# Optimization experiments

Hardware: AMD Instinct MI355X
Metric: run time of the kernel (lower is better)

## Reference

```python
import jax, jax.numpy as jnp
import numpy as np

N = 100000   # nodes
E = 1600000  # edges (before self-loops)
IN = 128     # in_features
H = 4        # heads
C = 64       # out_features per head
D = H * C    # concat output dim = 256
NEG_SLOPE = 0.2
EPS = 1e-5


def setup_inputs() -> dict:
    key = jax.random.key(0)
    k = jax.random.split(key, 8)
    x = jax.random.normal(k[0], (N, IN), jnp.float32)
    edge_index = jax.random.randint(k[1], (2, E), 0, N, jnp.int32)
    # GATConv params (glorot-ish init)
    W = jax.random.normal(k[2], (IN, D), jnp.float32) * np.float32(np.sqrt(2.0 / (IN + D)))
    att_src = jax.random.normal(k[3], (H, C), jnp.float32) * np.float32(np.sqrt(2.0 / C))
    att_dst = jax.random.normal(k[4], (H, C), jnp.float32) * np.float32(np.sqrt(2.0 / C))
    bias = jnp.zeros((D,), jnp.float32)
    # LayerNorm params
    gamma = jnp.ones((D,), jnp.float32)
    beta = jnp.zeros((D,), jnp.float32)
    return {"x": x, "edge_index": edge_index, "W": W, "att_src": att_src,
            "att_dst": att_dst, "bias": bias, "gamma": gamma, "beta": beta}


def reference(x, edge_index, W, att_src, att_dst, bias, gamma, beta):
    # --- GATConv (add_self_loops=True, negative_slope=0.2, eval-mode dropout) ---
    loops = jnp.arange(N, dtype=edge_index.dtype)
    ei = jnp.concatenate([edge_index, jnp.stack([loops, loops])], axis=1)  # (2, E+N)
    src, dst = ei[0], ei[1]

    h = (x @ W).reshape(N, H, C)                       # (N,H,C)
    a_s = jnp.einsum('nhc,hc->nh', h, att_src)          # (N,H)
    a_d = jnp.einsum('nhc,hc->nh', h, att_dst)          # (N,H)

    logits = jax.nn.leaky_relu(a_s[src] + a_d[dst], NEG_SLOPE)  # (Etot,H)
    # segment softmax over incoming edges of each destination node
    mx = jax.ops.segment_max(logits, dst, num_segments=N)       # (N,H)
    ex = jnp.exp(logits - mx[dst])
    den = jax.ops.segment_sum(ex, dst, num_segments=N)          # (N,H)
    alpha = ex / den[dst]                                       # (Etot,H)

    msg = h[src] * alpha[:, :, None]                             # (Etot,H,C)
    out = jax.ops.segment_sum(msg, dst, num_segments=N)          # (N,H,C)
    out = out.reshape(N, D) + bias

    # --- ELU + LayerNorm (dropout = identity in eval) ---
    out = jax.nn.elu(out)
    mu = out.mean(-1, keepdims=True)
    var = out.var(-1, keepdims=True)
    out = (out - mu) * jax.lax.rsqrt(var + EPS) * gamma + beta
    return out
```

## Files before the change

### kernel.cpp

```cpp
#include <hip/hip_runtime.h>
#include <hip/hip_bf16.h>

#define IN_F 128
#define DF   256
#define NEG  0.2f
#define LN_EPS 1e-5f

typedef __attribute__((ext_vector_type(8))) short bf16x8;
typedef __attribute__((ext_vector_type(4))) float f32x4;

__device__ __forceinline__ float lrelu(float x) { return x > 0.f ? x : NEG * x; }
__device__ __forceinline__ float b2f(unsigned short u) {
    union { unsigned int i; float f; } v; v.i = ((unsigned int)u) << 16; return v.f;
}
__device__ __forceinline__ unsigned short f2b(float f) {
    union { float f; unsigned int i; } v; v.f = f;
    unsigned int r = v.i + 0x7FFFu + ((v.i >> 16) & 1u);
    return (unsigned short)(r >> 16);
}

__global__ __launch_bounds__(256) void k_pack(const float* __restrict__ W,
                                              unsigned short* __restrict__ Wp)
{
    int t = blockIdx.x * 256 + threadIdx.x;
    if (t >= 16 * 4 * 64) return;
    int lane = t & 63, ks = (t >> 6) & 3, ct = t >> 8;
    int col = ct * 16 + (lane & 15);
    int kb  = ks * 32 + (lane >> 4) * 8;
    unsigned short* dst = Wp + (size_t)t * 8;
    #pragma unroll
    for (int j = 0; j < 8; ++j)
        dst[j] = f2b(W[(size_t)(kb + j) * DF + col]);
}

#define APAD 136
__global__ __launch_bounds__(256) void k_gemm(
        const float* __restrict__ x, const unsigned short* __restrict__ Wp,
        unsigned short* __restrict__ hb, int N)
{
    __shared__ unsigned short lds_a[64 * APAD];
    int t = threadIdx.x;
    int row0 = blockIdx.x * 64;

    const float4* xg = (const float4*)x;
    #pragma unroll
    for (int j = 0; j < 8; ++j) {
        int s = t + j * 256;
        int r = s >> 5, c4 = s & 31;
        ushort4 w = make_ushort4(0, 0, 0, 0);
        if (row0 + r < N) {
            float4 xv = xg[(size_t)(row0 + r) * 32 + c4];
            w = make_ushort4(f2b(xv.x), f2b(xv.y), f2b(xv.z), f2b(xv.w));
        }
        *(ushort4*)(&lds_a[r * APAD + c4 * 4]) = w;
    }
    __syncthreads();

    int lane = t & 63, wid = t >> 6;
    int rbase = (wid & 1) * 32;
    int cbase = (wid >> 1) * 128;
    int ct0 = cbase >> 4;

    bf16x8 af[2][4];
    #pragma unroll
    for (int rt = 0; rt < 2; ++rt)
        #pragma unroll
        for (int ks = 0; ks < 4; ++ks) {
            int r = rbase + rt * 16 + (lane & 15);
            int k = ks * 32 + (lane >> 4) * 8;
            af[rt][ks] = *(const bf16x8*)(&lds_a[r * APAD + k]);
        }

    f32x4 acc[2][8];
    #pragma unroll
    for (int rt = 0; rt < 2; ++rt)
        #pragma unroll
        for (int ct = 0; ct < 8; ++ct)
            acc[rt][ct] = (f32x4){0.f, 0.f, 0.f, 0.f};

    const bf16x8* Wp8 = (const bf16x8*)Wp;
    #pragma unroll
    for (int ct = 0; ct < 8; ++ct) {
        #pragma unroll
        for (int ks = 0; ks < 4; ++ks) {
            bf16x8 b = Wp8[((ct0 + ct) * 4 + ks) * 64 + lane];
            acc[0][ct] = __builtin_amdgcn_mfma_f32_16x16x32_bf16(af[0][ks], b, acc[0][ct], 0, 0, 0);
            acc[1][ct] = __builtin_amdgcn_mfma_f32_16x16x32_bf16(af[1][ks], b, acc[1][ct], 0, 0, 0);
        }
    }

    #pragma unroll
    for (int rt = 0; rt < 2; ++rt) {
        #pragma unroll
        for (int ct = 0; ct < 8; ++ct) {
            int col = cbase + ct * 16 + (lane & 15);
            #pragma unroll
            for (int r = 0; r < 4; ++r) {
                int row = row0 + rbase + rt * 16 + (lane >> 4) * 4 + r;
                if (row < N)
                    hb[(size_t)row * DF + col] = f2b(acc[rt][ct][r]);
            }
        }
    }
}

__global__ __launch_bounds__(256) void k_att(
        const unsigned short* __restrict__ hb,
        const float* __restrict__ att_s, const float* __restrict__ att_d,
        float* __restrict__ a_s, float* __restrict__ a_d, int N)
{
    int wid = threadIdx.x >> 6, lane = threadIdx.x & 63;
    int n = blockIdx.x * 4 + wid;
    if (n >= N) return;
    int d0 = lane << 2, head = lane >> 4;
    ushort4 hv = *(const ushort4*)(hb + (size_t)n * DF + d0);
    float4 as4 = *(const float4*)(att_s + d0);
    float4 ad4 = *(const float4*)(att_d + d0);
    float h0 = b2f(hv.x), h1 = b2f(hv.y), h2 = b2f(hv.z), h3 = b2f(hv.w);
    float vs = h0 * as4.x + h1 * as4.y + h2 * as4.z + h3 * as4.w;
    float vd = h0 * ad4.x + h1 * ad4.y + h2 * ad4.z + h3 * ad4.w;
    #pragma unroll
    for (int m = 8; m >= 1; m >>= 1) {
        vs += __shfl_xor(vs, m, 64);
        vd += __shfl_xor(vd, m, 64);
    }
    if ((lane & 15) == 0) {
        a_s[(size_t)n * 4 + head] = vs;
        a_d[(size_t)n * 4 + head] = vd;
    }
}

__global__ void k_count(const int* __restrict__ dste, int E, int* __restrict__ indeg)
{
    for (int e = blockIdx.x * blockDim.x + threadIdx.x; e < E; e += gridDim.x * blockDim.x)
        atomicAdd(&indeg[dste[e]], 1);
}

__global__ __launch_bounds__(256) void k_scanA(const int* __restrict__ indeg, int N, int* __restrict__ part)
{
    int t = threadIdx.x, base = blockIdx.x * 1024;
    int s = 0;
    #pragma unroll
    for (int j = 0; j < 4; ++j) { int i = base + t * 4 + j; if (i < N) s += indeg[i]; }
    #pragma unroll
    for (int m = 32; m >= 1; m >>= 1) s += __shfl_xor(s, m, 64);
    __shared__ int red[4];
    if ((t & 63) == 0) red[t >> 6] = s;
    __syncthreads();
    if (t == 0) part[blockIdx.x] = red[0] + red[1] + red[2] + red[3];
}

__global__ __launch_bounds__(128) void k_scanB(const int* __restrict__ part, int NB, int* __restrict__ bloff)
{
    __shared__ int buf[128];
    int t = threadIdx.x;
    int v = (t < NB) ? part[t] : 0;
    buf[t] = v;
    __syncthreads();
    for (int off = 1; off < 128; off <<= 1) {
        int x2 = (t >= off) ? buf[t - off] : 0;
        __syncthreads();
        buf[t] += x2;
        __syncthreads();
    }
    if (t < NB) bloff[t] = buf[t] - v;
}

__global__ __launch_bounds__(256) void k_scanC(const int* __restrict__ indeg, int N,
        const int* __restrict__ bloff, int* __restrict__ offs, int* __restrict__ cur)
{
    int t = threadIdx.x, bid = blockIdx.x, base = bid * 1024;
    int v[4]; int s = 0;
    #pragma unroll
    for (int j = 0; j < 4; ++j) { int i = base + t * 4 + j; v[j] = (i < N) ? indeg[i] : 0; s += v[j]; }
    __shared__ int lds[256];
    lds[t] = s;
    __syncthreads();
    for (int off = 1; off < 256; off <<= 1) {
        int x2 = (t >= off) ? lds[t - off] : 0;
        __syncthreads();
        lds[t] += x2;
        __syncthreads();
    }
    int run = lds[t] - s + bloff[bid];
    #pragma unroll
    for (int j = 0; j < 4; ++j) {
        int i = base + t * 4 + j;
        if (i < N) { offs[i] = run; cur[i] = run; }
        run += v[j];
    }
    if (bid == (int)gridDim.x - 1 && t == 255) offs[N] = run;
}

__global__ void k_scatter(const int* __restrict__ srce, const int* __restrict__ dste, int E,
                          int* __restrict__ cur, int* __restrict__ srclist)
{
    for (int e = blockIdx.x * blockDim.x + threadIdx.x; e < E; e += gridDim.x * blockDim.x) {
        int d = dste[e];
        int p = atomicAdd(&cur[d], 1);
        srclist[p] = srce[e];
    }
}

__global__ __launch_bounds__(256) void k_gather(
        const unsigned short* __restrict__ hb,
        const float* __restrict__ a_s, const float* __restrict__ a_d,
        const int* __restrict__ offs, const int* __restrict__ srclist,
        const float* __restrict__ bias, const float* __restrict__ gamma,
        const float* __restrict__ beta, float* __restrict__ out, int N)
{
    int wid = threadIdx.x >> 6, lane = threadIdx.x & 63;
    int n = blockIdx.x * 4 + wid;
    if (n >= N) return;
    int head = lane >> 4;
    int d0 = lane << 2;

    float adh = a_d[(size_t)n * 4 + head];
    int beg = offs[n], end = offs[n + 1];

    float acc0, acc1, acc2, acc3, den;
    {
        float as = a_s[(size_t)n * 4 + head];
        float p = expf(lrelu(as + adh));
        den = p;
        ushort4 hv = *(const ushort4*)(hb + (size_t)n * DF + d0);
        acc0 = p * b2f(hv.x); acc1 = p * b2f(hv.y);
        acc2 = p * b2f(hv.z); acc3 = p * b2f(hv.w);
    }

    int e = beg;
    int s_next = (e < end) ? srclist[e] : 0;
    while (e < end) {
        int s = s_next;
        ++e;
        if (e < end) s_next = srclist[e];
        float as = a_s[(size_t)s * 4 + head];
        ushort4 hv = *(const ushort4*)(hb + (size_t)s * DF + d0);
        float p = expf(lrelu(as + adh));
        den += p;
        acc0 = fmaf(p, b2f(hv.x), acc0); acc1 = fmaf(p, b2f(hv.y), acc1);
        acc2 = fmaf(p, b2f(hv.z), acc2); acc3 = fmaf(p, b2f(hv.w), acc3);
    }

    float inv = 1.f / den;
    float4 bia = *(const float4*)(bias + d0);
    float v0 = fmaf(acc0, inv, bia.x);
    float v1 = fmaf(acc1, inv, bia.y);
    float v2 = fmaf(acc2, inv, bia.z);
    float v3 = fmaf(acc3, inv, bia.w);
    v0 = v0 > 0.f ? v0 : expm1f(v0);
    v1 = v1 > 0.f ? v1 : expm1f(v1);
    v2 = v2 > 0.f ? v2 : expm1f(v2);
    v3 = v3 > 0.f ? v3 : expm1f(v3);

    float s1 = v0 + v1 + v2 + v3;
    float s2 = v0 * v0 + v1 * v1 + v2 * v2 + v3 * v3;
    #pragma unroll
    for (int m = 32; m >= 1; m >>= 1) {
        s1 += __shfl_xor(s1, m, 64);
        s2 += __shfl_xor(s2, m, 64);
    }
    float mu = s1 * (1.f / 256.f);
    float var = s2 * (1.f / 256.f) - mu * mu;
    float rs = rsqrtf(var + LN_EPS);
    float4 g  = *(const float4*)(gamma + d0);
    float4 be = *(const float4*)(beta + d0);
    float4 o;
    o.x = (v0 - mu) * rs * g.x + be.x;
    o.y = (v1 - mu) * rs * g.y + be.y;
    o.z = (v2 - mu) * rs * g.z + be.z;
    o.w = (v3 - mu) * rs * g.w + be.w;
    *(float4*)(out + (size_t)n * DF + d0) = o;
}

extern "C" void kernel_launch(void* const* d_in, const int* in_sizes, int n_in,
                              void* d_out, int out_size, void* d_ws, size_t ws_size,
                              hipStream_t stream)
{
    const float* x     = (const float*)d_in[0];
    const int*   ei    = (const int*)d_in[1];
    const float* W     = (const float*)d_in[2];
    const float* att_s = (const float*)d_in[3];
    const float* att_d = (const float*)d_in[4];
    const float* bias  = (const float*)d_in[5];
    const float* gamma = (const float*)d_in[6];
    const float* beta  = (const float*)d_in[7];
    float* out = (float*)d_out;

    int N = in_sizes[0] / IN_F;
    int E = in_sizes[1] / 2;
    const int* srce = ei;
    const int* dste = ei + E;

    char* wsb = (char*)d_ws;
    size_t off = 0;
    auto alloc = [&](size_t bytes) -> void* {
        void* p = wsb + off;
        off += (bytes + 255) & ~(size_t)255;
        return p;
    };
    unsigned short* hb = (unsigned short*)alloc((size_t)N * DF * sizeof(unsigned short));
    unsigned short* Wp = (unsigned short*)alloc((size_t)IN_F * DF * sizeof(unsigned short));
    float* a_s   = (float*)alloc((size_t)N * 4 * sizeof(float));
    float* a_d   = (float*)alloc((size_t)N * 4 * sizeof(float));
    int*   indeg = (int*)alloc((size_t)N * sizeof(int));
    int*   offs  = (int*)alloc(((size_t)N + 1) * sizeof(int));
    int*   cur   = (int*)alloc((size_t)N * sizeof(int));
    int*   srclist = (int*)alloc((size_t)E * sizeof(int));
    int NB = (N + 1023) / 1024;
    int* part  = (int*)alloc((size_t)NB * sizeof(int));
    int* bloff = (int*)alloc((size_t)NB * sizeof(int));

    (void)hipMemsetAsync(indeg, 0, (size_t)N * sizeof(int), stream);

    k_pack<<<16, 256, 0, stream>>>(W, Wp);
    k_gemm<<<(N + 63) / 64, 256, 0, stream>>>(x, Wp, hb, N);
    k_att<<<(N + 3) / 4, 256, 0, stream>>>(hb, att_s, att_d, a_s, a_d, N);
    k_count<<<2048, 256, 0, stream>>>(dste, E, indeg);
    k_scanA<<<NB, 256, 0, stream>>>(indeg, N, part);
    k_scanB<<<1, 128, 0, stream>>>(part, NB, bloff);
    k_scanC<<<NB, 256, 0, stream>>>(indeg, N, bloff, offs, cur);
    k_scatter<<<2048, 256, 0, stream>>>(srce, dste, E, cur, srclist);
    k_gather<<<(N + 3) / 4, 256, 0, stream>>>(hb, a_s, a_d, offs, srclist, bias, gamma, beta, out, N);
}
```

Before: 527.0 us.

## Batch edge logits across lanes and switch h storage to fp16

The gather kernel now handles incoming edges in batches of 16. Each lane loads one source index and computes its attention weight with fast __expf, then broadcasts the index and weight via shuffles for the feature accumulation, and the denominator is reduced with xor-shuffles. This removes the serial dependent index loads and the per-edge exp computed redundantly by every lane. The intermediate h buffer moves from bf16 to fp16, which gives more mantissa precision at the same size and changes the conversion instructions. The trade-off is extra shuffle traffic and lower occupancy in partial batches for low-degree nodes.

```diff
diff --git a/kernel.cpp b/kernel.cpp
--- a/kernel.cpp
+++ b/kernel.cpp
@@ -8,11 +8,10 @@
 
 typedef __attribute__((ext_vector_type(8))) short bf16x8;
 typedef __attribute__((ext_vector_type(4))) float f32x4;
+typedef _Float16 f16;
+typedef __attribute__((ext_vector_type(4))) _Float16 f16x4;
 
 __device__ __forceinline__ float lrelu(float x) { return x > 0.f ? x : NEG * x; }
-__device__ __forceinline__ float b2f(unsigned short u) {
-    union { unsigned int i; float f; } v; v.i = ((unsigned int)u) << 16; return v.f;
-}
 __device__ __forceinline__ unsigned short f2b(float f) {
     union { float f; unsigned int i; } v; v.f = f;
     unsigned int r = v.i + 0x7FFFu + ((v.i >> 16) & 1u);
@@ -36,7 +35,7 @@
 #define APAD 136
 __global__ __launch_bounds__(256) void k_gemm(
         const float* __restrict__ x, const unsigned short* __restrict__ Wp,
-        unsigned short* __restrict__ hb, int N)
+        f16* __restrict__ hb, int N)
 {
     __shared__ unsigned short lds_a[64 * APAD];
     int t = threadIdx.x;
@@ -98,14 +97,14 @@
             for (int r = 0; r < 4; ++r) {
                 int row = row0 + rbase + rt * 16 + (lane >> 4) * 4 + r;
                 if (row < N)
-                    hb[(size_t)row * DF + col] = f2b(acc[rt][ct][r]);
+                    hb[(size_t)row * DF + col] = (f16)acc[rt][ct][r];
             }
         }
     }
 }
 
 __global__ __launch_bounds__(256) void k_att(
-        const unsigned short* __restrict__ hb,
+        const f16* __restrict__ hb,
         const float* __restrict__ att_s, const float* __restrict__ att_d,
         float* __restrict__ a_s, float* __restrict__ a_d, int N)
 {
@@ -113,10 +112,10 @@
     int n = blockIdx.x * 4 + wid;
     if (n >= N) return;
     int d0 = lane << 2, head = lane >> 4;
-    ushort4 hv = *(const ushort4*)(hb + (size_t)n * DF + d0);
+    f16x4 hv = *(const f16x4*)(hb + (size_t)n * DF + d0);
     float4 as4 = *(const float4*)(att_s + d0);
     float4 ad4 = *(const float4*)(att_d + d0);
-    float h0 = b2f(hv.x), h1 = b2f(hv.y), h2 = b2f(hv.z), h3 = b2f(hv.w);
+    float h0 = (float)hv.x, h1 = (float)hv.y, h2 = (float)hv.z, h3 = (float)hv.w;
     float vs = h0 * as4.x + h1 * as4.y + h2 * as4.z + h3 * as4.w;
     float vd = h0 * ad4.x + h1 * ad4.y + h2 * ad4.z + h3 * ad4.w;
     #pragma unroll
@@ -203,7 +202,7 @@
 }
 
 __global__ __launch_bounds__(256) void k_gather(
-        const unsigned short* __restrict__ hb,
+        const f16* __restrict__ hb,
         const float* __restrict__ a_s, const float* __restrict__ a_d,
         const int* __restrict__ offs, const int* __restrict__ srclist,
         const float* __restrict__ bias, const float* __restrict__ gamma,
@@ -213,34 +212,43 @@
     int n = blockIdx.x * 4 + wid;
     if (n >= N) return;
     int head = lane >> 4;
+    int j16  = lane & 15;
     int d0 = lane << 2;
 
     float adh = a_d[(size_t)n * 4 + head];
     int beg = offs[n], end = offs[n + 1];
 
-    float acc0, acc1, acc2, acc3, den;
+    float acc0, acc1, acc2, acc3;
+    float den = 0.f;
     {
         float as = a_s[(size_t)n * 4 + head];
-        float p = expf(lrelu(as + adh));
-        den = p;
-        ushort4 hv = *(const ushort4*)(hb + (size_t)n * DF + d0);
-        acc0 = p * b2f(hv.x); acc1 = p * b2f(hv.y);
-        acc2 = p * b2f(hv.z); acc3 = p * b2f(hv.w);
-    }
-
-    int e = beg;
-    int s_next = (e < end) ? srclist[e] : 0;
-    while (e < end) {
-        int s = s_next;
-        ++e;
-        if (e < end) s_next = srclist[e];
+        float p = __expf(lrelu(as + adh));
+        if (j16 == 0) den = p;
+        f16x4 hv = *(const f16x4*)(hb + (size_t)n * DF + d0);
+        acc0 = p * (float)hv.x; acc1 = p * (float)hv.y;
+        acc2 = p * (float)hv.z; acc3 = p * (float)hv.w;
+    }
+
+    for (int tb = beg; tb < end; tb += 16) {
+        int nb = end - tb; nb = nb > 16 ? 16 : nb;
+        int   s = (j16 < nb) ? srclist[tb + j16] : 0;
         float as = a_s[(size_t)s * 4 + head];
-        ushort4 hv = *(const ushort4*)(hb + (size_t)s * DF + d0);
-        float p = expf(lrelu(as + adh));
+        float p  = (j16 < nb) ? __expf(lrelu(as + adh)) : 0.f;
         den += p;
-        acc0 = fmaf(p, b2f(hv.x), acc0); acc1 = fmaf(p, b2f(hv.y), acc1);
-        acc2 = fmaf(p, b2f(hv.z), acc2); acc3 = fmaf(p, b2f(hv.w), acc3);
-    }
+        #pragma unroll 2
+        for (int j = 0; j < nb; ++j) {
+            int   sj = __shfl(s, j, 64);
+            float pj = __shfl(p, (lane & 0x30) | j, 64);
+            f16x4 hv = *(const f16x4*)(hb + (size_t)sj * DF + d0);
+            acc0 = fmaf(pj, (float)hv.x, acc0);
+            acc1 = fmaf(pj, (float)hv.y, acc1);
+            acc2 = fmaf(pj, (float)hv.z, acc2);
+            acc3 = fmaf(pj, (float)hv.w, acc3);
+        }
+    }
+
+    #pragma unroll
+    for (int m = 8; m >= 1; m >>= 1) den += __shfl_xor(den, m, 64);
 
     float inv = 1.f / den;
     float4 bia = *(const float4*)(bias + d0);
@@ -299,7 +307,7 @@
         off += (bytes + 255) & ~(size_t)255;
         return p;
     };
-    unsigned short* hb = (unsigned short*)alloc((size_t)N * DF * sizeof(unsigned short));
+    f16* hb = (f16*)alloc((size_t)N * DF * sizeof(f16));
     unsigned short* Wp = (unsigned short*)alloc((size_t)IN_F * DF * sizeof(unsigned short));
     float* a_s   = (float*)alloc((size_t)N * 4 * sizeof(float));
     float* a_d   = (float*)alloc((size_t)N * 4 * sizeof(float));
```

New measurement: 526.7 us. Within noise of the previous version (-0.1%).
